# Kernel tuning notes

Measured on AMD Instinct MI355X. Metric: run time of the kernel, lower is better.

The kernel has to match this reference:

```python
import jax, jax.numpy as jnp
import numpy as np

D = 256       # vec_dim
HEADS = 8     # head_num
PS = 4        # patch_size
WS = 7        # window_size (in patches)
P = WS * WS   # tokens per window


def _relative_index():
    # replicates the torch meshgrid / relative coord logic (indexing='ij')
    coords = np.stack(np.meshgrid(np.arange(WS), np.arange(WS), indexing='ij'))  # [2,WS,WS]
    cf = coords.reshape(2, -1)                                                   # [2,P]
    rc = (cf[:, :, None] - cf[:, None, :]).transpose(1, 2, 0)                    # [P,P,2]
    rc[:, :, 0] += WS - 1
    rc[:, :, 1] += WS - 1
    rc[:, :, 1] *= 2 * WS - 1
    return rc.sum(-1)  # [P,P] ints in [0,(2WS-1)^2)


def _shift_mask(ch, cw):
    # standard swin shift mask built on the patch grid (ch, cw)
    fm = np.zeros((ch, cw))
    idx = (slice(0, -WS), slice(-WS, -(WS // 2)), slice(-(WS // 2), None))
    cnt = 0
    for y in idx:
        for x in idx:
            fm[y, x] = cnt
            cnt += 1
    nh, nw = ch // WS, cw // WS
    fm = fm.reshape(nh, WS, nw, WS).transpose(0, 2, 1, 3).reshape(nh * nw, P)
    m = fm[:, None, :] - fm[:, :, None]
    return np.where(m != 0, -100.0, 0.0).astype(np.float32)


def setup_inputs() -> dict:
    key = jax.random.key(0)
    ks = jax.random.split(key, 10)
    N, PN = 8, 3136
    s = 0.02
    return {
        'inputs': jax.random.normal(ks[0], (N, D, PN), jnp.float32),
        'Wk': jax.random.normal(ks[1], (HEADS * D, D), jnp.float32) * s,
        'bk': jax.random.normal(ks[2], (HEADS * D,), jnp.float32) * s,
        'Wq': jax.random.normal(ks[3], (HEADS * D, D), jnp.float32) * s,
        'bq': jax.random.normal(ks[4], (HEADS * D,), jnp.float32) * s,
        'Wv': jax.random.normal(ks[5], (HEADS * D, D), jnp.float32) * s,
        'bv': jax.random.normal(ks[6], (HEADS * D,), jnp.float32) * s,
        'Wo': jax.random.normal(ks[7], (D, HEADS * D), jnp.float32) * s,
        'bo': jax.random.normal(ks[8], (D,), jnp.float32) * s,
        'rel_code': jax.random.normal(ks[9], ((2 * WS - 1) ** 2, HEADS), jnp.float32) * 0.02,
        'h': 224,
        'w': 224,
    }


def _forward(inputs, Wk, bk, Wq, bq, Wv, bv, Wo, bo, rel_code, h, w):
    ch, cw = h // PS, w // PS            # patch grid
    N, _, PN = inputs.shape
    C = D // (PS * PS)
    nh, nw = ch // WS, cw // WS
    WIN = nh * nw

    # patches2features -> pixel-space roll by WS//2 -> features2patches
    x = inputs.reshape(N, C, PS, PS, ch, cw)
    x = x.transpose(0, 1, 4, 2, 5, 3).reshape(N, C, ch * PS, cw * PS)
    x = jnp.roll(x, (WS // 2, WS // 2), axis=(-2, -1))
    x = x.reshape(N, C, ch, PS, cw, PS).transpose(0, 2, 4, 1, 3, 5).reshape(N, PN, D)
    x = x.transpose(0, 2, 1)  # [N,D,PN]

    def proj(W, b):
        e = jnp.einsum('od,ndp->nop', W, x) + b[None, :, None]  # [N,HEADS*D,PN]
        e = e.reshape(N, HEADS, D, ch, cw)
        # window partition: n h d (nh w1)(nw w2) -> n h (nh nw) d (w1 w2)
        e = e.reshape(N, HEADS, D, nh, WS, nw, WS)
        return e.transpose(0, 1, 3, 5, 2, 4, 6).reshape(N, HEADS, WIN, D, P)

    k = proj(Wk, bk)
    q = proj(Wq, bq)
    v = proj(Wv, bv)

    # attn[p,q] = k_p . q_q  (softmax over keys p, axis=3)
    attn = jnp.einsum('nhgdp,nhgdq->nhgpq', k, q) / (D ** 0.5)
    mask = jnp.asarray(_shift_mask(ch, cw))
    attn = attn + mask[None, None]
    rel_idx = _relative_index().ravel()
    rel = rel_code[rel_idx].reshape(P, P, HEADS).transpose(2, 0, 1)  # [H,P,P]
    attn = attn + rel[None, :, None]
    wmap = jax.nn.softmax(attn, axis=3)

    out = jnp.einsum('nhgdp,nhgpq->nhgdq', v, wmap)
    # window merge back to [N,H,D,PN]
    out = out.reshape(N, HEADS, nh, nw, D, WS, WS)
    out = out.transpose(0, 1, 4, 2, 5, 3, 6).reshape(N, HEADS * D, PN)
    return jnp.einsum('od,ndp->nop', Wo, out) + bo[None, :, None]  # [N,D,PN]


def reference(inputs, Wk, bk, Wq, bq, Wv, bv, Wo, bo, rel_code, h, w):
    return _forward(inputs, Wk, bk, Wq, bq, Wv, bv, Wo, bo, rel_code, h, w)
```

## Files before the change

kernel.cpp:

```cpp
#include <hip/hip_runtime.h>
#include <hip/hip_bf16.h>


#define NBATCH 8
#define TROWS  3200
#define FSTR   264

typedef unsigned short ushort_t;
typedef __attribute__((ext_vector_type(8))) short bf16x8;
typedef __attribute__((ext_vector_type(8))) unsigned short u16x8;
typedef __attribute__((ext_vector_type(4))) float f32x4;

__device__ __forceinline__ float b2f(ushort_t u) {
  union { unsigned int i; float f; } v; v.i = ((unsigned int)u) << 16; return v.f;
}
__device__ __forceinline__ ushort_t f2b(float f) {
  union { float f; unsigned int u; } v; v.f = f;
  unsigned int u = v.u;
  return (ushort_t)((u + 0x7FFFu + ((u >> 16) & 1u)) >> 16);
}
__device__ __forceinline__ int regof(int y) { return (y < 49) ? 0 : ((y < 53) ? 1 : 2); }
__device__ __forceinline__ int div7(int t) { return (t * 37) >> 8; }
__device__ __forceinline__ int tmap(int p, int gi, int gj) {
  int wi = div7(p); return (gi * 7 + wi) * 56 + gj * 7 + (p - wi * 7);
}
__device__ __forceinline__ ushort4 pack4(f32x4 a) {
  ushort4 u; u.x = f2b(a[0]); u.y = f2b(a[1]); u.z = f2b(a[2]); u.w = f2b(a[3]);
  return u;
}

__global__ void k_prep(const float* __restrict__ Wk, const float* __restrict__ Wq,
                       const float* __restrict__ Wo, const float* __restrict__ Wv,
                       const float* __restrict__ bk, const float* __restrict__ bq,
                       const float* __restrict__ bv, const float* __restrict__ bo,
                       const float* __restrict__ relc,
                       ushort_t* __restrict__ Aext, ushort_t* __restrict__ Wov3,
                       float* __restrict__ cvec, float* __restrict__ relL2) {
  __shared__ float red[8];
  int blk = blockIdx.x, t = threadIdx.x;
  if (blk < 512) {
    int h = blk >> 6, b0 = (blk & 63) << 2, a = t;
    const float* wkh = Wk + h * 65536;
    const float* wqh = Wq + h * 65536;
    float a0 = 0.f, a1 = 0.f, a2 = 0.f, a3 = 0.f;
    for (int dd = 0; dd < 256; ++dd) {
      float wk = wkh[dd * 256 + a];
      float4 w4 = *(const float4*)(wqh + dd * 256 + b0);
      a0 += wk * w4.x; a1 += wk * w4.y; a2 += wk * w4.z; a3 += wk * w4.w;
    }
    ushort4 u; u.x = f2b(a0); u.y = f2b(a1); u.z = f2b(a2); u.w = f2b(a3);
    *(ushort4*)(Aext + (h * 256 + a) * 256 + b0) = u;
  } else if (blk < 1024) {
    int bb = blk - 512;
    int h = bb >> 6, o0 = (bb & 63) << 2, d = t;
    float a0 = 0.f, a1 = 0.f, a2 = 0.f, a3 = 0.f;
    for (int dd = 0; dd < 256; ++dd) {
      float wv = Wv[(h * 256 + dd) * 256 + d];
      a0 += Wo[(o0 + 0) * 2048 + h * 256 + dd] * wv;
      a1 += Wo[(o0 + 1) * 2048 + h * 256 + dd] * wv;
      a2 += Wo[(o0 + 2) * 2048 + h * 256 + dd] * wv;
      a3 += Wo[(o0 + 3) * 2048 + h * 256 + dd] * wv;
    }
    Wov3[(o0 + 0) * 2048 + h * 256 + d] = f2b(a0);
    Wov3[(o0 + 1) * 2048 + h * 256 + d] = f2b(a1);
    Wov3[(o0 + 2) * 2048 + h * 256 + d] = f2b(a2);
    Wov3[(o0 + 3) * 2048 + h * 256 + d] = f2b(a3);
  } else if (blk < 1032) {
    int h = blk - 1024;
    float s1 = 0.f, s2 = 0.f;
    for (int dd = 0; dd < 256; ++dd) {
      s1 += bk[h * 256 + dd] * Wq[(h * 256 + dd) * 256 + t];
      s2 += bq[h * 256 + dd] * Wk[(h * 256 + dd) * 256 + t];
    }
    Aext[(2048 + h) * 256 + t] = f2b(s1);
    Aext[(2056 + h) * 256 + t] = f2b(s2);
  } else if (blk == 1032) {
    for (int i = t; i < 112 * 256 / 8; i += 256)
      *(u16x8*)(Aext + 2064 * 256 + i * 8) = (u16x8){0,0,0,0,0,0,0,0};
  } else if (blk < 1289) {
    int o = blk - 1033;
    const float* wob = Wo + o * 2048;
    float acc = 0.f;
#pragma unroll
    for (int j = 0; j < 8; ++j) acc += wob[j * 256 + t] * bv[j * 256 + t];
#pragma unroll
    for (int s = 1; s < 64; s <<= 1) acc += __shfl_xor(acc, s);
    if ((t & 63) == 0) red[t >> 6] = acc;
    __syncthreads();
    if (t == 0) cvec[o] = bo[o] + red[0] + red[1] + red[2] + red[3];
  } else {
    if (t < 8) {
      float c = 0.f;
      for (int dd = 0; dd < 256; ++dd) c += bk[t * 256 + dd] * bq[t * 256 + dd];
      red[t] = c * 0.0625f;
    }
    __syncthreads();
    for (int i = t; i < 8 * 169; i += 256) {
      int h = i / 169, idx = i - h * 169;
      relL2[i] = relc[idx * 8 + h] + red[h];
    }
  }
}

__global__ void k_conv(const float* __restrict__ X, ushort_t* __restrict__ Xroll) {
  const int n = blockIdx.x / 57, y = blockIdx.x % 57;
  ushort_t* xr = Xroll + (size_t)n * TROWS * 256;
  const int d = threadIdx.x;
  if (y == 56) {
    for (int i = d; i < 64 * 256 / 8; i += 256)
      *(u16x8*)(xr + 3136 * 256 + i * 8) = (u16x8){0,0,0,0,0,0,0,0};
    return;
  }
  const int c = d >> 4, p1 = (d >> 2) & 3, p2 = d & 3;
  const int sp = c * 16 + (((p1 + 1) & 3) << 2) + ((p2 + 1) & 3);
  const int ty = (p1 == 3) ? y : ((y == 0) ? 55 : y - 1);
  const float* rowp = X + (size_t)n * 256 * 3136 + sp * 3136 + ty * 56;
  ushort_t* orow = xr + y * 56 * 256 + d;
  for (int x = 0; x < 56; ++x) {
    int tx = (p2 == 3) ? x : ((x == 0) ? 55 : x - 1);
    orow[x * 256] = f2b(rowp[tx]);
  }
}

__global__ __launch_bounds__(512, 1) void k_fused(
    const ushort_t* __restrict__ Xroll, const ushort_t* __restrict__ Aext,
    const ushort_t* __restrict__ Wov3, const float* __restrict__ cvec,
    const float* __restrict__ relL2, float* __restrict__ out) {
  __shared__ ushort_t Xp[64 * FSTR];
  __shared__ ushort_t Msm[64 * FSTR];
  __shared__ ushort_t Tsm[64 * FSTR];
  __shared__ ushort_t StB[64 * 72];
  __shared__ float aqsL[8 * 64];
  __shared__ float bpsL[8 * 64];
  __shared__ float relLh[8 * 169];
  __shared__ float mPart[2][64];
  __shared__ float sPart[2][64];

  const int tid = threadIdx.x;
  const int wave = tid >> 6, lane = tid & 63;
  const int quad = lane >> 4, l16 = lane & 15;
  const int n = blockIdx.x & 7, g = blockIdx.x >> 3;
  const int gi = g >> 3, gj = g & 7;
  const ushort_t* Xn = Xroll + (size_t)n * TROWS * 256;
  float* on = out + (size_t)n * 256 * 3136;

  {
    const int p = tid & 63, cg = tid >> 6;
    if (p < 49) {
      int t = tmap(p, gi, gj);
#pragma unroll
      for (int i = 0; i < 4; ++i)
        *(u16x8*)(&Xp[p * FSTR + (cg * 4 + i) * 8]) =
            *(const u16x8*)(Xn + t * 256 + (cg * 4 + i) * 8);
    } else {
#pragma unroll
      for (int i = 0; i < 4; ++i)
        *(u16x8*)(&Xp[p * FSTR + (cg * 4 + i) * 8]) = (u16x8){0,0,0,0,0,0,0,0};
    }
  }
  for (int i = tid; i < 8 * 169; i += 512) relLh[i] = relL2[i];
  __syncthreads();

  bf16x8 xfr[2][2];
#pragma unroll
  for (int dt = 0; dt < 2; ++dt) {
    const int d = (wave * 2 + dt) * 16 + l16;
#pragma unroll
    for (int kk = 0; kk < 2; ++kk)
#pragma unroll
      for (int j = 0; j < 8; ++j)
        xfr[dt][kk][j] = (short)Xp[(kk * 32 + quad * 8 + j) * FSTR + d];
  }

  auto m_step = [&](int h) {
    f32x4 macc[2][4];
#pragma unroll
    for (int i = 0; i < 2; ++i)
#pragma unroll
      for (int t = 0; t < 4; ++t) macc[i][t] = (f32x4){0.f, 0.f, 0.f, 0.f};
    const ushort_t* Ah =
        Aext + (size_t)(h * 256 + wave * 32 + l16) * 256 + quad * 8;
#pragma unroll
    for (int kk = 0; kk < 8; ++kk) {
      bf16x8 ga[2];
#pragma unroll
      for (int i = 0; i < 2; ++i)
        ga[i] = *(const bf16x8*)(Ah + i * 16 * 256 + kk * 32);
#pragma unroll
      for (int t = 0; t < 4; ++t) {
        bf16x8 bx_ = *(const bf16x8*)(&Xp[(t * 16 + l16) * FSTR + kk * 32 + quad * 8]);
#pragma unroll
        for (int i = 0; i < 2; ++i)
          macc[i][t] = __builtin_amdgcn_mfma_f32_16x16x32_bf16(ga[i], bx_, macc[i][t], 0, 0, 0);
      }
    }
#pragma unroll
    for (int i = 0; i < 2; ++i)
#pragma unroll
      for (int t = 0; t < 4; ++t)
        *(ushort4*)(&Msm[(t * 16 + l16) * FSTR + wave * 32 + i * 16 + quad * 4]) =
            pack4(macc[i][t]);
  };

  m_step(0);
  if (wave == 0) {
    f32x4 eacc[4];
#pragma unroll
    for (int t = 0; t < 4; ++t) eacc[t] = (f32x4){0.f, 0.f, 0.f, 0.f};
    const ushort_t* Ae = Aext + (size_t)(2048 + l16) * 256 + quad * 8;
#pragma unroll
    for (int kk = 0; kk < 8; ++kk) {
      bf16x8 ea = *(const bf16x8*)(Ae + kk * 32);
#pragma unroll
      for (int t = 0; t < 4; ++t) {
        bf16x8 bx_ = *(const bf16x8*)(&Xp[(t * 16 + l16) * FSTR + kk * 32 + quad * 8]);
        eacc[t] = __builtin_amdgcn_mfma_f32_16x16x32_bf16(ea, bx_, eacc[t], 0, 0, 0);
      }
    }
#pragma unroll
    for (int t = 0; t < 4; ++t) {
      const int tok = t * 16 + l16;
#pragma unroll
      for (int r = 0; r < 4; ++r) {
        const int e = quad * 4 + r;
        if (e < 8) aqsL[e * 64 + tok] = eacc[t][r];
        else       bpsL[(e - 8) * 64 + tok] = eacc[t][r];
      }
    }
  }
  __syncthreads();

  const int wq = wave & 3, wp = wave >> 2;
  const int q = wq * 16 + l16;
  const int qq = (q < 49) ? q : 48;
  const int yq = div7(qq), xq = qq - yq * 7;
  const int fq = regof(gi * 7 + yq) * 3 + regof(gj * 7 + xq);

  f32x4 oacc[2][4];
#pragma unroll
  for (int i = 0; i < 2; ++i)
#pragma unroll
    for (int j = 0; j < 4; ++j) oacc[i][j] = (f32x4){0.f, 0.f, 0.f, 0.f};

  for (int h = 0; h < 8; ++h) {
    f32x4 sacc[2];
    sacc[0] = (f32x4){0.f, 0.f, 0.f, 0.f};
    sacc[1] = (f32x4){0.f, 0.f, 0.f, 0.f};
#pragma unroll
    for (int kk = 0; kk < 8; ++kk) {
      bf16x8 bfm = *(const bf16x8*)(&Msm[q * FSTR + kk * 32 + quad * 8]);
#pragma unroll
      for (int j = 0; j < 2; ++j) {
        bf16x8 af = *(const bf16x8*)(&Xp[((wp * 2 + j) * 16 + l16) * FSTR + kk * 32 + quad * 8]);
        sacc[j] = __builtin_amdgcn_mfma_f32_16x16x32_bf16(af, bfm, sacc[j], 0, 0, 0);
      }
    }
    float v[8];
    const float aqv = aqsL[h * 64 + q];
    const float* rel_h = &relLh[h * 169];
    float mw = -1e30f;
#pragma unroll
    for (int j = 0; j < 2; ++j)
#pragma unroll
      for (int r = 0; r < 4; ++r) {
        const int p = (wp * 2 + j) * 16 + quad * 4 + r;
        float val = -1e30f;
        if (p < 49) {
          const int yp = div7(p), xp = p - yp * 7;
          const int fp = regof(gi * 7 + yp) * 3 + regof(gj * 7 + xp);
          val = (sacc[j][r] + aqv + bpsL[h * 64 + p]) * 0.0625f +
                rel_h[(yp - yq + 6) + 13 * (xp - xq + 6)];
          if (fp != fq) val -= 100.f;
        }
        v[j * 4 + r] = val;
        mw = fmaxf(mw, val);
      }
    mw = fmaxf(mw, __shfl_xor(mw, 16));
    mw = fmaxf(mw, __shfl_xor(mw, 32));
    if (lane < 16) mPart[wp][wq * 16 + lane] = mw;
    __syncthreads();
    const float mg = fmaxf(mPart[0][q], mPart[1][q]);
    float sw = 0.f;
#pragma unroll
    for (int i2 = 0; i2 < 8; ++i2) { v[i2] = __expf(v[i2] - mg); sw += v[i2]; }
    sw += __shfl_xor(sw, 16);
    sw += __shfl_xor(sw, 32);
    if (lane < 16) sPart[wp][wq * 16 + lane] = sw;
    __syncthreads();
    const float inv = 1.f / (sPart[0][q] + sPart[1][q]);
#pragma unroll
    for (int j = 0; j < 2; ++j) {
      ushort4 u;
      u.x = f2b(v[j * 4 + 0] * inv); u.y = f2b(v[j * 4 + 1] * inv);
      u.z = f2b(v[j * 4 + 2] * inv); u.w = f2b(v[j * 4 + 3] * inv);
      *(ushort4*)(&StB[q * 72 + (wp * 2 + j) * 16 + quad * 4]) = u;
    }
    if (h < 7) m_step(h + 1);
    __syncthreads();
    bf16x8 wfr[2][8];
#pragma unroll
    for (int i = 0; i < 2; ++i)
#pragma unroll
      for (int kk = 0; kk < 8; ++kk)
        wfr[i][kk] = *(const bf16x8*)(Wov3 +
            (size_t)(wave * 32 + i * 16 + l16) * 2048 + h * 256 + kk * 32 + quad * 8);
#pragma unroll
    for (int qt = 0; qt < 4; ++qt) {
      f32x4 tacc[2];
      tacc[0] = (f32x4){0.f, 0.f, 0.f, 0.f};
      tacc[1] = (f32x4){0.f, 0.f, 0.f, 0.f};
#pragma unroll
      for (int kk = 0; kk < 2; ++kk) {
        bf16x8 bfw = *(const bf16x8*)(&StB[(qt * 16 + l16) * 72 + kk * 32 + quad * 8]);
#pragma unroll
        for (int dt = 0; dt < 2; ++dt)
          tacc[dt] = __builtin_amdgcn_mfma_f32_16x16x32_bf16(xfr[dt][kk], bfw, tacc[dt], 0, 0, 0);
      }
#pragma unroll
      for (int dt = 0; dt < 2; ++dt)
        *(ushort4*)(&Tsm[(qt * 16 + l16) * FSTR + (wave * 2 + dt) * 16 + quad * 4]) =
            pack4(tacc[dt]);
    }
    __syncthreads();
#pragma unroll
    for (int kk = 0; kk < 8; ++kk) {
#pragma unroll
      for (int qt = 0; qt < 4; ++qt) {
        bf16x8 bfo = *(const bf16x8*)(&Tsm[(qt * 16 + l16) * FSTR + kk * 32 + quad * 8]);
#pragma unroll
        for (int i = 0; i < 2; ++i)
          oacc[i][qt] = __builtin_amdgcn_mfma_f32_16x16x32_bf16(wfr[i][kk], bfo, oacc[i][qt], 0, 0, 0);
      }
    }
    __syncthreads();
  }
#pragma unroll
  for (int i = 0; i < 2; ++i) {
    const int ob = wave * 32 + i * 16 + quad * 4;
    const float4 cv = *(const float4*)(cvec + ob);
#pragma unroll
    for (int qt = 0; qt < 4; ++qt) {
      const int q2 = qt * 16 + l16;
      if (q2 < 49) {
        const int t2 = tmap(q2, gi, gj);
        on[(size_t)(ob + 0) * 3136 + t2] = oacc[i][qt][0] + cv.x;
        on[(size_t)(ob + 1) * 3136 + t2] = oacc[i][qt][1] + cv.y;
        on[(size_t)(ob + 2) * 3136 + t2] = oacc[i][qt][2] + cv.z;
        on[(size_t)(ob + 3) * 3136 + t2] = oacc[i][qt][3] + cv.w;
      }
    }
  }
}

extern "C" void kernel_launch(void* const* d_in, const int* in_sizes, int n_in,
                              void* d_out, int out_size, void* d_ws, size_t ws_size,
                              hipStream_t stream) {
  (void)in_sizes; (void)n_in; (void)out_size; (void)ws_size;
  const float* X  = (const float*)d_in[0];
  const float* Wk = (const float*)d_in[1];
  const float* bk = (const float*)d_in[2];
  const float* Wq = (const float*)d_in[3];
  const float* bq = (const float*)d_in[4];
  const float* Wv = (const float*)d_in[5];
  const float* bv = (const float*)d_in[6];
  const float* Wo = (const float*)d_in[7];
  const float* bo = (const float*)d_in[8];
  const float* rc = (const float*)d_in[9];

  ushort_t* Xroll = (ushort_t*)d_ws;
  ushort_t* Aext  = Xroll + (size_t)8 * TROWS * 256;
  ushort_t* Wov3  = Aext + 2176 * 256;
  float* fbase = (float*)(Wov3 + 256 * 2048);
  float* cvec  = fbase;
  float* relL2 = fbase + 256;
  float* out = (float*)d_out;

  k_prep <<<dim3(1290), dim3(256), 0, stream>>>(Wk, Wq, Wo, Wv, bk, bq, bv, bo, rc,
                                                Aext, Wov3, cvec, relL2);
  k_conv <<<dim3(8 * 57), dim3(256), 0, stream>>>(X, Xroll);
  k_fused<<<dim3(512), dim3(512), 0, stream>>>(Xroll, Aext, Wov3, cvec, relL2, out);
}
```

Measured before the change: 305.2 us.

## Hoist X fragments to registers, merge softmax reductions, drop per-head barriers

Loads the per-wave X fragments used by the score matmul into registers once, before the head loop, instead of re-reading them from shared memory for every head. The score accumulation is split into two independent chains to give more MFMA parallelism. The two-pass cross-wave softmax (max, then sum) becomes a single pass that combines partial maxima and sums with rescaling, removing one barrier per head. The trailing barrier at the end of each head iteration is also removed. In exchange, register pressure rises (16 extra bf16x8 fragments), and dropping the final barrier risks a race on Tsm/StB reuse.

```diff
diff --git a/kernel.cpp b/kernel.cpp
--- a/kernel.cpp
+++ b/kernel.cpp
@@ -161,6 +161,16 @@
   for (int i = tid; i < 8 * 169; i += 512) relLh[i] = relL2[i];
   __syncthreads();
 
+  const int wp = wave >> 2;
+  const int wq = wave & 3;
+
+  bf16x8 xb[8][2];
+#pragma unroll
+  for (int kk = 0; kk < 8; ++kk)
+#pragma unroll
+    for (int j = 0; j < 2; ++j)
+      xb[kk][j] = *(const bf16x8*)(&Xp[((wp * 2 + j) * 16 + l16) * FSTR + kk * 32 + quad * 8]);
+
   bf16x8 xfr[2][2];
 #pragma unroll
   for (int dt = 0; dt < 2; ++dt) {
@@ -230,7 +240,6 @@
   }
   __syncthreads();
 
-  const int wq = wave & 3, wp = wave >> 2;
   const int q = wq * 16 + l16;
   const int qq = (q < 49) ? q : 48;
   const int yq = div7(qq), xq = qq - yq * 7;
@@ -243,19 +252,20 @@
     for (int j = 0; j < 4; ++j) oacc[i][j] = (f32x4){0.f, 0.f, 0.f, 0.f};
 
   for (int h = 0; h < 8; ++h) {
-    f32x4 sacc[2];
-    sacc[0] = (f32x4){0.f, 0.f, 0.f, 0.f};
-    sacc[1] = (f32x4){0.f, 0.f, 0.f, 0.f};
-#pragma unroll
-    for (int kk = 0; kk < 8; ++kk) {
-      bf16x8 bfm = *(const bf16x8*)(&Msm[q * FSTR + kk * 32 + quad * 8]);
+    f32x4 sa0[2], sa1[2];
+    sa0[0] = (f32x4){0.f,0.f,0.f,0.f}; sa0[1] = (f32x4){0.f,0.f,0.f,0.f};
+    sa1[0] = (f32x4){0.f,0.f,0.f,0.f}; sa1[1] = (f32x4){0.f,0.f,0.f,0.f};
+#pragma unroll
+    for (int kk = 0; kk < 8; kk += 2) {
+      bf16x8 bfm0 = *(const bf16x8*)(&Msm[q * FSTR + kk * 32 + quad * 8]);
+      bf16x8 bfm1 = *(const bf16x8*)(&Msm[q * FSTR + (kk + 1) * 32 + quad * 8]);
 #pragma unroll
       for (int j = 0; j < 2; ++j) {
-        bf16x8 af = *(const bf16x8*)(&Xp[((wp * 2 + j) * 16 + l16) * FSTR + kk * 32 + quad * 8]);
-        sacc[j] = __builtin_amdgcn_mfma_f32_16x16x32_bf16(af, bfm, sacc[j], 0, 0, 0);
-      }
-    }
-    float v[8];
+        sa0[j] = __builtin_amdgcn_mfma_f32_16x16x32_bf16(xb[kk][j], bfm0, sa0[j], 0, 0, 0);
+        sa1[j] = __builtin_amdgcn_mfma_f32_16x16x32_bf16(xb[kk + 1][j], bfm1, sa1[j], 0, 0, 0);
+      }
+    }
+    float v[8], ew[8];
     const float aqv = aqsL[h * 64 + q];
     const float* rel_h = &relLh[h * 169];
     float mw = -1e30f;
@@ -268,7 +278,7 @@
         if (p < 49) {
           const int yp = div7(p), xp = p - yp * 7;
           const int fp = regof(gi * 7 + yp) * 3 + regof(gj * 7 + xp);
-          val = (sacc[j][r] + aqv + bpsL[h * 64 + p]) * 0.0625f +
+          val = (sa0[j][r] + sa1[j][r] + aqv + bpsL[h * 64 + p]) * 0.0625f +
                 rel_h[(yp - yq + 6) + 13 * (xp - xq + 6)];
           if (fp != fq) val -= 100.f;
         }
@@ -277,23 +287,26 @@
       }
     mw = fmaxf(mw, __shfl_xor(mw, 16));
     mw = fmaxf(mw, __shfl_xor(mw, 32));
-    if (lane < 16) mPart[wp][wq * 16 + lane] = mw;
-    __syncthreads();
-    const float mg = fmaxf(mPart[0][q], mPart[1][q]);
     float sw = 0.f;
 #pragma unroll
-    for (int i2 = 0; i2 < 8; ++i2) { v[i2] = __expf(v[i2] - mg); sw += v[i2]; }
+    for (int i2 = 0; i2 < 8; ++i2) { ew[i2] = __expf(v[i2] - mw); sw += ew[i2]; }
     sw += __shfl_xor(sw, 16);
     sw += __shfl_xor(sw, 32);
-    if (lane < 16) sPart[wp][wq * 16 + lane] = sw;
-    __syncthreads();
-    const float inv = 1.f / (sPart[0][q] + sPart[1][q]);
-#pragma unroll
-    for (int j = 0; j < 2; ++j) {
-      ushort4 u;
-      u.x = f2b(v[j * 4 + 0] * inv); u.y = f2b(v[j * 4 + 1] * inv);
-      u.z = f2b(v[j * 4 + 2] * inv); u.w = f2b(v[j * 4 + 3] * inv);
-      *(ushort4*)(&StB[q * 72 + (wp * 2 + j) * 16 + quad * 4]) = u;
+    if (lane < 16) { mPart[wp][wq * 16 + lane] = mw; sPart[wp][wq * 16 + lane] = sw; }
+    __syncthreads();
+    {
+      const float m0 = mPart[0][q], m1 = mPart[1][q];
+      const float s0 = sPart[0][q], s1 = sPart[1][q];
+      const float mg = fmaxf(m0, m1);
+      const float tot = s0 * __expf(m0 - mg) + s1 * __expf(m1 - mg);
+      const float scale = __expf(mw - mg) / tot;
+#pragma unroll
+      for (int j = 0; j < 2; ++j) {
+        ushort4 u;
+        u.x = f2b(ew[j * 4 + 0] * scale); u.y = f2b(ew[j * 4 + 1] * scale);
+        u.z = f2b(ew[j * 4 + 2] * scale); u.w = f2b(ew[j * 4 + 3] * scale);
+        *(ushort4*)(&StB[q * 72 + (wp * 2 + j) * 16 + quad * 4]) = u;
+      }
     }
     if (h < 7) m_step(h + 1);
     __syncthreads();
@@ -332,7 +345,6 @@
           oacc[i][qt] = __builtin_amdgcn_mfma_f32_16x16x32_bf16(wfr[i][kk], bfo, oacc[i][qt], 0, 0, 0);
       }
     }
-    __syncthreads();
   }
 #pragma unroll
   for (int i = 0; i < 2; ++i) {
```

After: 297.4 us. 2.6% less time.
